# Performance work log

Hardware: AMD Instinct MI355X
Metric: run time of the kernel (lower is better)

## Reference

```python
import jax, jax.numpy as jnp
import numpy as np

NUM_USERS = 100000
NUM_ITEMS = 50000
EMB_DIM = 64
NUM_EDGES = 2000000


def setup_inputs() -> dict:
    key = jax.random.key(0)
    k1, k2, k3, k4 = jax.random.split(key, 4)
    user_table = jax.random.normal(k1, (NUM_USERS, EMB_DIM), dtype=jnp.float32) * 0.1
    item_table = jax.random.normal(k2, (NUM_ITEMS, EMB_DIM), dtype=jnp.float32) * 0.1
    user_idx = jax.random.randint(k3, (NUM_EDGES,), 0, NUM_USERS, dtype=jnp.int32)
    item_idx = jax.random.randint(k4, (NUM_EDGES,), 0, NUM_ITEMS, dtype=jnp.int32)
    return {"user_table": user_table, "item_table": item_table,
            "user_idx": user_idx, "item_idx": item_idx, "num_layers": 3}


def reference(user_table, item_table, user_idx, item_idx, num_layers):
    """LightGCN-style k-hop propagation over a sparse bipartite user-item graph.

    A_hat[u,i] = 1/sqrt(deg_u * deg_i); emb_out = mean over hops 0..K of A_hat^k @ emb_0.
    Returns concatenated [num_users+num_items, d] embeddings (forward() then slices).
    """
    n_users, d = user_table.shape
    n_items = item_table.shape[0]
    ones = jnp.ones(user_idx.shape[0], dtype=user_table.dtype)
    deg_u = jax.ops.segment_sum(ones, user_idx, num_segments=n_users)
    deg_i = jax.ops.segment_sum(ones, item_idx, num_segments=n_items)
    deg_u = jnp.where(deg_u > 0, deg_u, 1.0)
    deg_i = jnp.where(deg_i > 0, deg_i, 1.0)
    # per-edge symmetric normalization coefficient [E]
    norm = jax.lax.rsqrt(deg_u[user_idx] * deg_i[item_idx])

    u, it = user_table, item_table
    acc_u, acc_i = u, it
    for _ in range(num_layers):
        # messages: item -> user and user -> item (gather + weighted scatter-add)
        msg_u = jax.ops.segment_sum(norm[:, None] * it[item_idx], user_idx, num_segments=n_users)
        msg_i = jax.ops.segment_sum(norm[:, None] * u[user_idx], item_idx, num_segments=n_items)
        u, it = msg_u, msg_i
        acc_u = acc_u + u
        acc_i = acc_i + it
    scale = 1.0 / (num_layers + 1)
    return jnp.concatenate([acc_u * scale, acc_i * scale], axis=0)
```

## Files before the change

### kernel.cpp

```cpp
#include <hip/hip_runtime.h>
#include <hip/hip_fp16.h>
#include <stdint.h>

#define NU 100000
#define NI 50000
#define NN (NU + NI)
#define DIM 64
#define NE 2000000
#define TOT (NN * DIM)

#define NBU 782
#define NBI 782
#define NBKT (NBU + NBI)
#define SCAP 3064
#define CGRP 25
#define NC 63
#define CCAP 67584

#define BEPT1 4
#define BCH1 (256 * BEPT1)
#define BG1 ((NE + BCH1 - 1) / BCH1)
#define KB2 17

typedef float f4v __attribute__((ext_vector_type(4)));
typedef float f2v __attribute__((ext_vector_type(2)));

__device__ __forceinline__ int bucket_r0(int b) {
    return (b < NBU) ? (b << 7) : (NU + ((b - NBU) << 6));
}


__global__ void bin1_kernel(const int* __restrict__ uidx, const int* __restrict__ iidx,
                            int* __restrict__ ccur, uint32_t* __restrict__ cstg) {
    __shared__ int cnt[NC];
    __shared__ int base[NC + 1];
    __shared__ int gbase[NC];
    __shared__ uint32_t rec[2 * BCH1];
    __shared__ uint8_t cid[2 * BCH1];
    int tid = threadIdx.x;
    for (int i = tid; i < NC; i += 256) cnt[i] = 0;
    __syncthreads();

    uint32_t pk[2 * BEPT1]; int cs[2 * BEPT1]; int rk[2 * BEPT1];
    int t0 = blockIdx.x * BCH1 + tid;
#pragma unroll
    for (int k = 0; k < BEPT1; ++k) {
        int e = t0 + k * 256;
        bool ok = e < NE;
        int u = ok ? __builtin_nontemporal_load(uidx + e) : 0;
        int itm = ok ? __builtin_nontemporal_load(iidx + e) : 0;
        int b = u >> 7; int c = b / 25; int f5 = b - c * 25;
        pk[2 * k] = ((uint32_t)f5 << 23) | ((uint32_t)(u & 127) << 16) | (uint32_t)itm;
        cs[2 * k] = ok ? c : -1;
        int b2 = NBU + (itm >> 6); int c2 = b2 / 25; int f52 = b2 - c2 * 25;
        pk[2 * k + 1] = ((uint32_t)f52 << 23) | ((uint32_t)(itm & 63) << 17) | (uint32_t)u;
        cs[2 * k + 1] = ok ? c2 : -1;
    }
#pragma unroll
    for (int k = 0; k < 2 * BEPT1; ++k)
        rk[k] = (cs[k] >= 0) ? atomicAdd(&cnt[cs[k]], 1) : 0;
    __syncthreads();
    if (tid == 0) {
        int s = 0;
        for (int i = 0; i < NC; ++i) { base[i] = s; s += cnt[i]; }
        base[NC] = s;
    }
    __syncthreads();
    for (int i = tid; i < NC; i += 256)
        if (cnt[i] > 0) gbase[i] = atomicAdd(&ccur[i], cnt[i]);
#pragma unroll
    for (int k = 0; k < 2 * BEPT1; ++k)
        if (cs[k] >= 0) {
            int p = base[cs[k]] + rk[k];
            rec[p] = pk[k];
            cid[p] = (uint8_t)cs[k];
        }
    __syncthreads();
    int T = base[NC];
    for (int p = tid; p < T; p += 256) {
        int c = cid[p];
        int pos = gbase[c] + (p - base[c]);
        if (pos < CCAP)
            __builtin_nontemporal_store(rec[p], cstg + (size_t)c * CCAP + pos);
    }
}

__global__ void bin2_kernel(const int* __restrict__ ccnt, const uint32_t* __restrict__ cstg,
                            int* __restrict__ bktcur, uint32_t* __restrict__ stg) {
    int c = blockIdx.x / KB2;
    int sl = blockIdx.x % KB2;
    int n = min(ccnt[c], CCAP);
    int lo = sl * 4096;
    if (lo >= n) return;
    int hi = min(lo + 4096, n);
    int m = hi - lo;
    __shared__ int cnt[CGRP];
    __shared__ int base[CGRP + 1];
    __shared__ int gbase[CGRP];
    __shared__ uint32_t rec[4096];
    int tid = threadIdx.x;
    if (tid < CGRP) cnt[tid] = 0;
    __syncthreads();

    uint32_t pk[16]; int fa[16]; int rk[16];
    const uint32_t* run = cstg + (size_t)c * CCAP + lo;
#pragma unroll
    for (int k = 0; k < 16; ++k) {
        int p = tid + k * 256;
        bool ok = p < m;
        uint32_t r = ok ? __builtin_nontemporal_load(run + p) : 0;
        pk[k] = r;
        fa[k] = ok ? (int)(r >> 23) : -1;
    }
#pragma unroll
    for (int k = 0; k < 16; ++k)
        rk[k] = (fa[k] >= 0) ? atomicAdd(&cnt[fa[k]], 1) : 0;
    __syncthreads();
    if (tid == 0) {
        int s = 0;
        for (int i = 0; i < CGRP; ++i) { base[i] = s; s += cnt[i]; }
        base[CGRP] = s;
    }
    __syncthreads();
    if (tid < CGRP && cnt[tid] > 0)
        gbase[tid] = atomicAdd(&bktcur[c * CGRP + tid], cnt[tid]);
#pragma unroll
    for (int k = 0; k < 16; ++k)
        if (fa[k] >= 0) rec[base[fa[k]] + rk[k]] = pk[k];
    __syncthreads();
    int T = base[CGRP];
    for (int p = tid; p < T; p += 256) {
        uint32_t r = rec[p];
        int f5 = r >> 23;
        int pos = gbase[f5] + (p - base[f5]);
        if (pos < SCAP)
            __builtin_nontemporal_store(r, stg + (size_t)(c * CGRP + f5) * SCAP + pos);
    }
}

__global__ void placeA_kernel(const int* __restrict__ bktcnt, const uint32_t* __restrict__ stg,
                              int* __restrict__ deg) {
    __shared__ int rowcnt[128];
    int b = blockIdx.x;
    int tid = threadIdx.x;
    int r0 = bucket_r0(b);
    int r1 = (b < NBU) ? min(r0 + 128, NU) : min(r0 + 64, NN);
    int nrows = r1 - r0;
    if (tid < nrows) rowcnt[tid] = 0;
    __syncthreads();
    int n = min(bktcnt[b], SCAP);
    const uint32_t* run = stg + (size_t)b * SCAP;
    bool isU = b < NBU;
    for (int p = tid; p < n; p += 256) {
        uint32_t r = __builtin_nontemporal_load(run + p);
        int row = isU ? ((r >> 16) & 0x7F) : ((r >> 17) & 0x3F);
        atomicAdd(&rowcnt[row], 1);
    }
    __syncthreads();
    if (tid < nrows) deg[r0 + tid] = rowcnt[tid];
}

__global__ void scan1_kernel(const int* __restrict__ deg, int* __restrict__ incl,
                             int* __restrict__ bsum) {
    __shared__ int tmp[256];
    int i = blockIdx.x * 256 + threadIdx.x;
    int v = (i < NN) ? deg[i] : 0;
    tmp[threadIdx.x] = v;
    __syncthreads();
    for (int off = 1; off < 256; off <<= 1) {
        int t = (threadIdx.x >= off) ? tmp[threadIdx.x - off] : 0;
        __syncthreads();
        tmp[threadIdx.x] += t;
        __syncthreads();
    }
    if (i < NN) incl[i] = tmp[threadIdx.x];
    if (threadIdx.x == 255) bsum[blockIdx.x] = tmp[255];
}

__global__ void scan2_kernel(int* __restrict__ bsum, int nb) {
    __shared__ int tmp[1024];
    int v = (threadIdx.x < nb) ? bsum[threadIdx.x] : 0;
    tmp[threadIdx.x] = v;
    __syncthreads();
    for (int off = 1; off < 1024; off <<= 1) {
        int t = (threadIdx.x >= off) ? tmp[threadIdx.x - off] : 0;
        __syncthreads();
        tmp[threadIdx.x] += t;
        __syncthreads();
    }
    if (threadIdx.x < nb) bsum[threadIdx.x] = tmp[threadIdx.x] - v;
}

__global__ void scan3_kernel(const int* __restrict__ deg, const int* __restrict__ incl,
                             const int* __restrict__ bsum,
                             int* __restrict__ rowptr, float* __restrict__ rdeg,
                             float* __restrict__ irdeg) {
    int i = blockIdx.x * 256 + threadIdx.x;
    if (i >= NN) return;
    int inc = incl[i] + bsum[blockIdx.x];
    rowptr[i + 1] = inc;
    int d = deg[i];
    rdeg[i] = (d > 0) ? rsqrtf((float)d) : 1.0f;
    irdeg[i] = (d > 0) ? sqrtf((float)d) : 1.0f;
    if (i == 0) rowptr[0] = 0;
}

__global__ void placeB_kernel(const int* __restrict__ rowptr, const int* __restrict__ bktcnt,
                              const uint32_t* __restrict__ stg, int* __restrict__ nbrs) {
    __shared__ int rptr[129];
    __shared__ int rowcnt[128];
    __shared__ int outb[SCAP];
    int b = blockIdx.x;
    int tid = threadIdx.x;
    int r0 = bucket_r0(b);
    int r1 = (b < NBU) ? min(r0 + 128, NU) : min(r0 + 64, NN);
    int nrows = r1 - r0;
    if (tid <= nrows) rptr[tid] = rowptr[r0 + tid];
    if (tid < nrows) rowcnt[tid] = 0;
    __syncthreads();
    int lo = rptr[0];
    int n = min(bktcnt[b], SCAP);
    const uint32_t* run = stg + (size_t)b * SCAP;
    bool isU = b < NBU;
    for (int p = tid; p < n; p += 256) {
        uint32_t r = __builtin_nontemporal_load(run + p);
        int row = isU ? ((r >> 16) & 0x7F) : ((r >> 17) & 0x3F);
        int nbr = isU ? (NU + (int)(r & 0xFFFF)) : (int)(r & 0x1FFFF);
        int rk = atomicAdd(&rowcnt[row], 1);
        outb[rptr[row] - lo + rk] = nbr;
    }
    __syncthreads();
    int nseg = rptr[nrows] - lo;
    for (int i = tid; i < nseg; i += 256)
        __builtin_nontemporal_store(outb[i], nbrs + lo + i);
}


__global__ void initsrc_kernel(const float* __restrict__ ut, const float* __restrict__ it,
                               const float* __restrict__ rdeg, __half* __restrict__ srcH) {
    int i = blockIdx.x * blockDim.x + threadIdx.x;
    const int NU4 = NU * DIM / 4;
    const int T4 = TOT / 4;
    if (i >= T4) return;
    float4 v = (i < NU4) ? ((const float4*)ut)[i] : ((const float4*)it)[i - NU4];
    float r = rdeg[i >> 4];
    union { __half2 h2[2]; f2v v2; } u;
    u.h2[0] = __floats2half2_rn(r * v.x, r * v.y);
    u.h2[1] = __floats2half2_rn(r * v.z, r * v.w);
    *((f2v*)(srcH + (size_t)i * 4)) = u.v2;
}

__global__ void gather_kernel(const int* __restrict__ rowptr, const int* __restrict__ nbrs,
                              const float* __restrict__ rdeg,
                              const __half* __restrict__ srcH, __half* __restrict__ nxtH) {
    int wid = (int)(((unsigned)blockIdx.x * blockDim.x + threadIdx.x) >> 6);
    if (wid >= NN) return;
    int lane = threadIdx.x & 63;
    int g = lane >> 3;
    int c = lane & 7;
    int start = rowptr[wid];
    int end = rowptr[wid + 1];
    int deg = end - start;

    int nb_l = (lane < deg) ? __builtin_nontemporal_load(nbrs + start + lane) : 0;

    float s0=0,s1=0,s2=0,s3=0,s4=0,s5=0,s6=0,s7=0;
    int dmain = deg < 64 ? deg : 64;
    int iters = (dmain + 7) >> 3;
    for (int t = 0; t < iters; ++t) {
        int idx = t * 8 + g;
        int nb = __shfl(nb_l, idx & 63, 64);
        bool ok = idx < dmain;
        if (!ok) nb = 0;
        union { f4v v; __half2 h2[4]; } u;
        u.v = *((const f4v*)(srcH + (size_t)nb * DIM) + c);
        if (ok) {
            float2 f0 = __half22float2(u.h2[0]);
            float2 f1 = __half22float2(u.h2[1]);
            float2 f2 = __half22float2(u.h2[2]);
            float2 f3 = __half22float2(u.h2[3]);
            s0 += f0.x; s1 += f0.y; s2 += f1.x; s3 += f1.y;
            s4 += f2.x; s5 += f2.y; s6 += f3.x; s7 += f3.y;
        }
    }
    for (int k = start + 64 + g; k < end; k += 8) {
        int nb = nbrs[k];
        union { f4v v; __half2 h2[4]; } u;
        u.v = *((const f4v*)(srcH + (size_t)nb * DIM) + c);
        float2 f0 = __half22float2(u.h2[0]);
        float2 f1 = __half22float2(u.h2[1]);
        float2 f2 = __half22float2(u.h2[2]);
        float2 f3 = __half22float2(u.h2[3]);
        s0 += f0.x; s1 += f0.y; s2 += f1.x; s3 += f1.y;
        s4 += f2.x; s5 += f2.y; s6 += f3.x; s7 += f3.y;
    }
#pragma unroll
    for (int mask = 8; mask <= 32; mask <<= 1) {
        s0 += __shfl_xor(s0, mask, 64); s1 += __shfl_xor(s1, mask, 64);
        s2 += __shfl_xor(s2, mask, 64); s3 += __shfl_xor(s3, mask, 64);
        s4 += __shfl_xor(s4, mask, 64); s5 += __shfl_xor(s5, mask, 64);
        s6 += __shfl_xor(s6, mask, 64); s7 += __shfl_xor(s7, mask, 64);
    }
    if (lane < 8) {
        float r = rdeg[wid];
        float w = r * r;
        union { f4v v; __half2 h2[4]; } o;
        o.h2[0] = __floats2half2_rn(w * s0, w * s1);
        o.h2[1] = __floats2half2_rn(w * s2, w * s3);
        o.h2[2] = __floats2half2_rn(w * s4, w * s5);
        o.h2[3] = __floats2half2_rn(w * s6, w * s7);
        __builtin_nontemporal_store(o.v, (f4v*)(nxtH + (size_t)wid * DIM + c * 8));
    }
}

__global__ void gather_fused_kernel(const int* __restrict__ rowptr, const int* __restrict__ nbrs,
                                    const float* __restrict__ rdeg, const float* __restrict__ irdeg,
                                    const __half* __restrict__ srcH,
                                    const __half* __restrict__ n1, const __half* __restrict__ n2,
                                    const float* __restrict__ ut, const float* __restrict__ it,
                                    float* __restrict__ acc) {
    int wid = (int)(((unsigned)blockIdx.x * blockDim.x + threadIdx.x) >> 6);
    if (wid >= NN) return;
    int lane = threadIdx.x & 63;
    int g = lane >> 3;
    int c = lane & 7;
    int start = rowptr[wid];
    int end = rowptr[wid + 1];
    int deg = end - start;

    int nb_l = (lane < deg) ? __builtin_nontemporal_load(nbrs + start + lane) : 0;

    float s0=0,s1=0,s2=0,s3=0,s4=0,s5=0,s6=0,s7=0;
    int dmain = deg < 64 ? deg : 64;
    int iters = (dmain + 7) >> 3;
    for (int t = 0; t < iters; ++t) {
        int idx = t * 8 + g;
        int nb = __shfl(nb_l, idx & 63, 64);
        bool ok = idx < dmain;
        if (!ok) nb = 0;
        union { f4v v; __half2 h2[4]; } u;
        u.v = *((const f4v*)(srcH + (size_t)nb * DIM) + c);
        if (ok) {
            float2 f0 = __half22float2(u.h2[0]);
            float2 f1 = __half22float2(u.h2[1]);
            float2 f2 = __half22float2(u.h2[2]);
            float2 f3 = __half22float2(u.h2[3]);
            s0 += f0.x; s1 += f0.y; s2 += f1.x; s3 += f1.y;
            s4 += f2.x; s5 += f2.y; s6 += f3.x; s7 += f3.y;
        }
    }
    for (int k = start + 64 + g; k < end; k += 8) {
        int nb = nbrs[k];
        union { f4v v; __half2 h2[4]; } u;
        u.v = *((const f4v*)(srcH + (size_t)nb * DIM) + c);
        float2 f0 = __half22float2(u.h2[0]);
        float2 f1 = __half22float2(u.h2[1]);
        float2 f2 = __half22float2(u.h2[2]);
        float2 f3 = __half22float2(u.h2[3]);
        s0 += f0.x; s1 += f0.y; s2 += f1.x; s3 += f1.y;
        s4 += f2.x; s5 += f2.y; s6 += f3.x; s7 += f3.y;
    }
#pragma unroll
    for (int mask = 8; mask <= 32; mask <<= 1) {
        s0 += __shfl_xor(s0, mask, 64); s1 += __shfl_xor(s1, mask, 64);
        s2 += __shfl_xor(s2, mask, 64); s3 += __shfl_xor(s3, mask, 64);
        s4 += __shfl_xor(s4, mask, 64); s5 += __shfl_xor(s5, mask, 64);
        s6 += __shfl_xor(s6, mask, 64); s7 += __shfl_xor(s7, mask, 64);
    }
    if (lane < 8) {
        float r = rdeg[wid];
        float w = irdeg[wid];
        const float* e0 = ((wid < NU) ? (ut + (size_t)wid * DIM)
                                      : (it + (size_t)(wid - NU) * DIM)) + c * 8;
        f4v ea = ((const f4v*)e0)[0];
        f4v eb = ((const f4v*)e0)[1];
        union { f4v v; __half2 h2[4]; } a1, a2;
        size_t ro = (size_t)wid * DIM + c * 8;
        a1.v = __builtin_nontemporal_load((const f4v*)(n1 + ro));
        a2.v = __builtin_nontemporal_load((const f4v*)(n2 + ro));
        f4v oa, ob;
        float2 f1 = __half22float2(a1.h2[0]), f2 = __half22float2(a2.h2[0]);
        oa.x = 0.25f * (ea.x + w * (f1.x + f2.x) + r * s0);
        oa.y = 0.25f * (ea.y + w * (f1.y + f2.y) + r * s1);
        f1 = __half22float2(a1.h2[1]); f2 = __half22float2(a2.h2[1]);
        oa.z = 0.25f * (ea.z + w * (f1.x + f2.x) + r * s2);
        oa.w = 0.25f * (ea.w + w * (f1.y + f2.y) + r * s3);
        f1 = __half22float2(a1.h2[2]); f2 = __half22float2(a2.h2[2]);
        ob.x = 0.25f * (eb.x + w * (f1.x + f2.x) + r * s4);
        ob.y = 0.25f * (eb.y + w * (f1.y + f2.y) + r * s5);
        f1 = __half22float2(a1.h2[3]); f2 = __half22float2(a2.h2[3]);
        ob.z = 0.25f * (eb.z + w * (f1.x + f2.x) + r * s6);
        ob.w = 0.25f * (eb.w + w * (f1.y + f2.y) + r * s7);
        __builtin_nontemporal_store(oa, (f4v*)(acc + ro));
        __builtin_nontemporal_store(ob, (f4v*)(acc + ro) + 1);
    }
}

extern "C" void kernel_launch(void* const* d_in, const int* in_sizes, int n_in,
                              void* d_out, int out_size, void* d_ws, size_t ws_size,
                              hipStream_t stream) {
    const float* ut = (const float*)d_in[0];
    const float* it = (const float*)d_in[1];
    const int* uidx = (const int*)d_in[2];
    const int* iidx = (const int*)d_in[3];

    float* acc = (float*)d_out;

    int* wsi = (int*)d_ws;
    int* deg    = wsi;
    int* incl   = deg + NN;
    int* rowptr = incl + NN;
    int* bsum   = rowptr + (NN + 1);
    float* rdeg = (float*)(bsum + 1024);
    float* irdeg = rdeg + NN;
    int* bktcur = (int*)(irdeg + NN);
    int* ccur   = bktcur + NBKT;
    size_t off = (size_t)((int*)(ccur + NC) - wsi);
    off = (off + 15) & ~(size_t)15;
    int* nbrs   = wsi + off;
    __half* bufA = (__half*)(nbrs + 2 * (size_t)NE);
    __half* bufB = bufA + (size_t)TOT;
    __half* bufC = bufB + (size_t)TOT;
    uint32_t* stg  = (uint32_t*)bufA;
    uint32_t* cstg = (uint32_t*)bufB;

    const int B = 256;
    const int nb = (NN + 255) / 256;

    hipMemsetAsync(bktcur, 0, sizeof(int) * (NBKT + NC), stream);
    bin1_kernel<<<BG1, 256, 0, stream>>>(uidx, iidx, ccur, cstg);
    bin2_kernel<<<NC * KB2, 256, 0, stream>>>(ccur, cstg, bktcur, stg);
    placeA_kernel<<<NBKT, 256, 0, stream>>>(bktcur, stg, deg);
    scan1_kernel<<<nb, 256, 0, stream>>>(deg, incl, bsum);
    scan2_kernel<<<1, 1024, 0, stream>>>(bsum, nb);
    scan3_kernel<<<nb, 256, 0, stream>>>(deg, incl, bsum, rowptr, rdeg, irdeg);
    placeB_kernel<<<NBKT, 256, 0, stream>>>(rowptr, bktcur, stg, nbrs);

    initsrc_kernel<<<(TOT / 4 + B - 1) / B, B, 0, stream>>>(ut, it, rdeg, bufA);

    const int gblocks = NN / 4;
    gather_kernel<<<gblocks, B, 0, stream>>>(rowptr, nbrs, rdeg, bufA, bufB);
    gather_kernel<<<gblocks, B, 0, stream>>>(rowptr, nbrs, rdeg, bufB, bufC);
    gather_fused_kernel<<<gblocks, B, 0, stream>>>(rowptr, nbrs, rdeg, irdeg,
                                                   bufC, bufB, bufC, ut, it, acc);
}
```

Before: 416.3 us.

## Fuse degree count and row-pointer scan into bucket placement, unroll gather loads

The per-row degree count, three-stage prefix scan and neighbour placement are replaced by one single-block scan over bucket counts plus one placement kernel. That kernel counts rows in shared memory, computes local offsets and writes rowptr, rdeg and irdeg itself, removing four launches and a global pass over the degree arrays. The gather loop is moved into a shared helper that issues four independent neighbour-row loads per step with separate accumulators, to raise memory-level parallelism. The final kernel now reads the layer-0 embedding from the fp16 scaled buffer instead of the fp32 tables, which adds fp16 rounding to the hop-0 term.

```diff
diff --git a/kernel.cpp b/kernel.cpp
--- a/kernel.cpp
+++ b/kernel.cpp
@@ -138,76 +138,38 @@
     }
 }
 
-__global__ void placeA_kernel(const int* __restrict__ bktcnt, const uint32_t* __restrict__ stg,
-                              int* __restrict__ deg) {
-    __shared__ int rowcnt[128];
-    int b = blockIdx.x;
+__global__ void scanB_kernel(const int* __restrict__ bktcnt, int* __restrict__ bktbase) {
+    __shared__ int partial[256];
     int tid = threadIdx.x;
-    int r0 = bucket_r0(b);
-    int r1 = (b < NBU) ? min(r0 + 128, NU) : min(r0 + 64, NN);
-    int nrows = r1 - r0;
-    if (tid < nrows) rowcnt[tid] = 0;
-    __syncthreads();
-    int n = min(bktcnt[b], SCAP);
-    const uint32_t* run = stg + (size_t)b * SCAP;
-    bool isU = b < NBU;
-    for (int p = tid; p < n; p += 256) {
-        uint32_t r = __builtin_nontemporal_load(run + p);
-        int row = isU ? ((r >> 16) & 0x7F) : ((r >> 17) & 0x3F);
-        atomicAdd(&rowcnt[row], 1);
-    }
-    __syncthreads();
-    if (tid < nrows) deg[r0 + tid] = rowcnt[tid];
-}
-
-__global__ void scan1_kernel(const int* __restrict__ deg, int* __restrict__ incl,
-                             int* __restrict__ bsum) {
-    __shared__ int tmp[256];
-    int i = blockIdx.x * 256 + threadIdx.x;
-    int v = (i < NN) ? deg[i] : 0;
-    tmp[threadIdx.x] = v;
+    int loc[7];
+    int s = 0;
+#pragma unroll
+    for (int k = 0; k < 7; ++k) {
+        int i = tid * 7 + k;
+        loc[k] = (i < NBKT) ? min(bktcnt[i], SCAP) : 0;
+        s += loc[k];
+    }
+    partial[tid] = s;
     __syncthreads();
     for (int off = 1; off < 256; off <<= 1) {
-        int t = (threadIdx.x >= off) ? tmp[threadIdx.x - off] : 0;
+        int v = (tid >= off) ? partial[tid - off] : 0;
         __syncthreads();
-        tmp[threadIdx.x] += t;
+        partial[tid] += v;
         __syncthreads();
     }
-    if (i < NN) incl[i] = tmp[threadIdx.x];
-    if (threadIdx.x == 255) bsum[blockIdx.x] = tmp[255];
-}
-
-__global__ void scan2_kernel(int* __restrict__ bsum, int nb) {
-    __shared__ int tmp[1024];
-    int v = (threadIdx.x < nb) ? bsum[threadIdx.x] : 0;
-    tmp[threadIdx.x] = v;
-    __syncthreads();
-    for (int off = 1; off < 1024; off <<= 1) {
-        int t = (threadIdx.x >= off) ? tmp[threadIdx.x - off] : 0;
-        __syncthreads();
-        tmp[threadIdx.x] += t;
-        __syncthreads();
-    }
-    if (threadIdx.x < nb) bsum[threadIdx.x] = tmp[threadIdx.x] - v;
-}
-
-__global__ void scan3_kernel(const int* __restrict__ deg, const int* __restrict__ incl,
-                             const int* __restrict__ bsum,
-                             int* __restrict__ rowptr, float* __restrict__ rdeg,
-                             float* __restrict__ irdeg) {
-    int i = blockIdx.x * 256 + threadIdx.x;
-    if (i >= NN) return;
-    int inc = incl[i] + bsum[blockIdx.x];
-    rowptr[i + 1] = inc;
-    int d = deg[i];
-    rdeg[i] = (d > 0) ? rsqrtf((float)d) : 1.0f;
-    irdeg[i] = (d > 0) ? sqrtf((float)d) : 1.0f;
-    if (i == 0) rowptr[0] = 0;
-}
-
-__global__ void placeB_kernel(const int* __restrict__ rowptr, const int* __restrict__ bktcnt,
-                              const uint32_t* __restrict__ stg, int* __restrict__ nbrs) {
-    __shared__ int rptr[129];
+    int excl = (tid == 0) ? 0 : partial[tid - 1];
+#pragma unroll
+    for (int k = 0; k < 7; ++k) {
+        int i = tid * 7 + k;
+        if (i < NBKT) { bktbase[i] = excl; excl += loc[k]; }
+    }
+    if (tid == 255) bktbase[NBKT] = partial[255];
+}
+
+__global__ void placeB2_kernel(const int* __restrict__ bktbase, const uint32_t* __restrict__ stg,
+                               int* __restrict__ rowptr, float* __restrict__ rdeg,
+                               float* __restrict__ irdeg, int* __restrict__ nbrs) {
+    __shared__ int rowstart[129];
     __shared__ int rowcnt[128];
     __shared__ int outb[SCAP];
     int b = blockIdx.x;
@@ -215,23 +177,42 @@
     int r0 = bucket_r0(b);
     int r1 = (b < NBU) ? min(r0 + 128, NU) : min(r0 + 64, NN);
     int nrows = r1 - r0;
-    if (tid <= nrows) rptr[tid] = rowptr[r0 + tid];
+    int lo = bktbase[b];
+    int n = bktbase[b + 1] - lo;
     if (tid < nrows) rowcnt[tid] = 0;
     __syncthreads();
-    int lo = rptr[0];
-    int n = min(bktcnt[b], SCAP);
     const uint32_t* run = stg + (size_t)b * SCAP;
     bool isU = b < NBU;
     for (int p = tid; p < n; p += 256) {
         uint32_t r = __builtin_nontemporal_load(run + p);
         int row = isU ? ((r >> 16) & 0x7F) : ((r >> 17) & 0x3F);
+        atomicAdd(&rowcnt[row], 1);
+    }
+    __syncthreads();
+    if (tid == 0) {
+        int s = 0;
+        for (int i = 0; i < nrows; ++i) { rowstart[i] = s; s += rowcnt[i]; }
+        rowstart[nrows] = s;
+    }
+    __syncthreads();
+    if (tid < nrows) {
+        int d = rowcnt[tid];
+        rowptr[r0 + tid] = lo + rowstart[tid];
+        rdeg[r0 + tid] = (d > 0) ? rsqrtf((float)d) : 1.0f;
+        irdeg[r0 + tid] = (d > 0) ? sqrtf((float)d) : 1.0f;
+        rowcnt[tid] = 0;
+    }
+    if (b == NBKT - 1 && tid == 0) rowptr[NN] = lo + n;
+    __syncthreads();
+    for (int p = tid; p < n; p += 256) {
+        uint32_t r = __builtin_nontemporal_load(run + p);
+        int row = isU ? ((r >> 16) & 0x7F) : ((r >> 17) & 0x3F);
         int nbr = isU ? (NU + (int)(r & 0xFFFF)) : (int)(r & 0x1FFFF);
         int rk = atomicAdd(&rowcnt[row], 1);
-        outb[rptr[row] - lo + rk] = nbr;
-    }
-    __syncthreads();
-    int nseg = rptr[nrows] - lo;
-    for (int i = tid; i < nseg; i += 256)
+        outb[rowstart[row] + rk] = nbr;
+    }
+    __syncthreads();
+    for (int i = tid; i < n; i += 256)
         __builtin_nontemporal_store(outb[i], nbrs + lo + i);
 }
 
@@ -250,6 +231,108 @@
     *((f2v*)(srcH + (size_t)i * 4)) = u.v2;
 }
 
+__device__ __forceinline__ void gather_core(const int* __restrict__ rowptr,
+                                            const int* __restrict__ nbrs,
+                                            const __half* __restrict__ srcH,
+                                            int wid, int lane, int g, int c,
+                                            float* out) {
+    int start = rowptr[wid];
+    int end = rowptr[wid + 1];
+    int deg = end - start;
+    int nb_l = (lane < deg) ? __builtin_nontemporal_load(nbrs + start + lane) : 0;
+    float acc[4][8];
+#pragma unroll
+    for (int j = 0; j < 4; ++j)
+#pragma unroll
+        for (int k = 0; k < 8; ++k) acc[j][k] = 0.f;
+    int dmain = deg < 64 ? deg : 64;
+    int iters = (dmain + 7) >> 3;
+    int t = 0;
+    for (; t + 4 <= iters; t += 4) {
+        int nb[4]; bool ok[4];
+#pragma unroll
+        for (int j = 0; j < 4; ++j) {
+            int idx = (t + j) * 8 + g;
+            nb[j] = __shfl(nb_l, idx & 63, 64);
+            ok[j] = idx < dmain;
+            if (!ok[j]) nb[j] = 0;
+        }
+        union { f4v v; __half2 h2[4]; } u[4];
+#pragma unroll
+        for (int j = 0; j < 4; ++j)
+            u[j].v = *((const f4v*)(srcH + (size_t)nb[j] * DIM) + c);
+#pragma unroll
+        for (int j = 0; j < 4; ++j)
+            if (ok[j]) {
+#pragma unroll
+                for (int h = 0; h < 4; ++h) {
+                    float2 f = __half22float2(u[j].h2[h]);
+                    acc[j][2 * h] += f.x; acc[j][2 * h + 1] += f.y;
+                }
+            }
+    }
+    if (t + 2 <= iters) {
+        int nb[2]; bool ok[2];
+#pragma unroll
+        for (int j = 0; j < 2; ++j) {
+            int idx = (t + j) * 8 + g;
+            nb[j] = __shfl(nb_l, idx & 63, 64);
+            ok[j] = idx < dmain;
+            if (!ok[j]) nb[j] = 0;
+        }
+        union { f4v v; __half2 h2[4]; } u[2];
+#pragma unroll
+        for (int j = 0; j < 2; ++j)
+            u[j].v = *((const f4v*)(srcH + (size_t)nb[j] * DIM) + c);
+#pragma unroll
+        for (int j = 0; j < 2; ++j)
+            if (ok[j]) {
+#pragma unroll
+                for (int h = 0; h < 4; ++h) {
+                    float2 f = __half22float2(u[j].h2[h]);
+                    acc[j][2 * h] += f.x; acc[j][2 * h + 1] += f.y;
+                }
+            }
+        t += 2;
+    }
+    if (t < iters) {
+        int idx = t * 8 + g;
+        int nb0 = __shfl(nb_l, idx & 63, 64);
+        bool ok0 = idx < dmain;
+        if (!ok0) nb0 = 0;
+        union { f4v v; __half2 h2[4]; } u0;
+        u0.v = *((const f4v*)(srcH + (size_t)nb0 * DIM) + c);
+        if (ok0) {
+#pragma unroll
+            for (int h = 0; h < 4; ++h) {
+                float2 f = __half22float2(u0.h2[h]);
+                acc[0][2 * h] += f.x; acc[0][2 * h + 1] += f.y;
+            }
+        }
+    }
+    for (int k = start + 64 + g; k < end; k += 8) {
+        int nb = nbrs[k];
+        union { f4v v; __half2 h2[4]; } u0;
+        u0.v = *((const f4v*)(srcH + (size_t)nb * DIM) + c);
+#pragma unroll
+        for (int h = 0; h < 4; ++h) {
+            float2 f = __half22float2(u0.h2[h]);
+            acc[0][2 * h] += f.x; acc[0][2 * h + 1] += f.y;
+        }
+    }
+    float s[8];
+#pragma unroll
+    for (int k = 0; k < 8; ++k)
+        s[k] = acc[0][k] + acc[1][k] + acc[2][k] + acc[3][k];
+#pragma unroll
+    for (int mask = 8; mask <= 32; mask <<= 1) {
+#pragma unroll
+        for (int k = 0; k < 8; ++k) s[k] += __shfl_xor(s[k], mask, 64);
+    }
+#pragma unroll
+    for (int k = 0; k < 8; ++k) out[k] = s[k];
+}
+
 __global__ void gather_kernel(const int* __restrict__ rowptr, const int* __restrict__ nbrs,
                               const float* __restrict__ rdeg,
                               const __half* __restrict__ srcH, __half* __restrict__ nxtH) {
@@ -258,57 +341,16 @@
     int lane = threadIdx.x & 63;
     int g = lane >> 3;
     int c = lane & 7;
-    int start = rowptr[wid];
-    int end = rowptr[wid + 1];
-    int deg = end - start;
-
-    int nb_l = (lane < deg) ? __builtin_nontemporal_load(nbrs + start + lane) : 0;
-
-    float s0=0,s1=0,s2=0,s3=0,s4=0,s5=0,s6=0,s7=0;
-    int dmain = deg < 64 ? deg : 64;
-    int iters = (dmain + 7) >> 3;
-    for (int t = 0; t < iters; ++t) {
-        int idx = t * 8 + g;
-        int nb = __shfl(nb_l, idx & 63, 64);
-        bool ok = idx < dmain;
-        if (!ok) nb = 0;
-        union { f4v v; __half2 h2[4]; } u;
-        u.v = *((const f4v*)(srcH + (size_t)nb * DIM) + c);
-        if (ok) {
-            float2 f0 = __half22float2(u.h2[0]);
-            float2 f1 = __half22float2(u.h2[1]);
-            float2 f2 = __half22float2(u.h2[2]);
-            float2 f3 = __half22float2(u.h2[3]);
-            s0 += f0.x; s1 += f0.y; s2 += f1.x; s3 += f1.y;
-            s4 += f2.x; s5 += f2.y; s6 += f3.x; s7 += f3.y;
-        }
-    }
-    for (int k = start + 64 + g; k < end; k += 8) {
-        int nb = nbrs[k];
-        union { f4v v; __half2 h2[4]; } u;
-        u.v = *((const f4v*)(srcH + (size_t)nb * DIM) + c);
-        float2 f0 = __half22float2(u.h2[0]);
-        float2 f1 = __half22float2(u.h2[1]);
-        float2 f2 = __half22float2(u.h2[2]);
-        float2 f3 = __half22float2(u.h2[3]);
-        s0 += f0.x; s1 += f0.y; s2 += f1.x; s3 += f1.y;
-        s4 += f2.x; s5 += f2.y; s6 += f3.x; s7 += f3.y;
-    }
-#pragma unroll
-    for (int mask = 8; mask <= 32; mask <<= 1) {
-        s0 += __shfl_xor(s0, mask, 64); s1 += __shfl_xor(s1, mask, 64);
-        s2 += __shfl_xor(s2, mask, 64); s3 += __shfl_xor(s3, mask, 64);
-        s4 += __shfl_xor(s4, mask, 64); s5 += __shfl_xor(s5, mask, 64);
-        s6 += __shfl_xor(s6, mask, 64); s7 += __shfl_xor(s7, mask, 64);
-    }
+    float s[8];
+    gather_core(rowptr, nbrs, srcH, wid, lane, g, c, s);
     if (lane < 8) {
         float r = rdeg[wid];
         float w = r * r;
         union { f4v v; __half2 h2[4]; } o;
-        o.h2[0] = __floats2half2_rn(w * s0, w * s1);
-        o.h2[1] = __floats2half2_rn(w * s2, w * s3);
-        o.h2[2] = __floats2half2_rn(w * s4, w * s5);
-        o.h2[3] = __floats2half2_rn(w * s6, w * s7);
+        o.h2[0] = __floats2half2_rn(w * s[0], w * s[1]);
+        o.h2[1] = __floats2half2_rn(w * s[2], w * s[3]);
+        o.h2[2] = __floats2half2_rn(w * s[4], w * s[5]);
+        o.h2[3] = __floats2half2_rn(w * s[6], w * s[7]);
         __builtin_nontemporal_store(o.v, (f4v*)(nxtH + (size_t)wid * DIM + c * 8));
     }
 }
@@ -316,81 +358,36 @@
 __global__ void gather_fused_kernel(const int* __restrict__ rowptr, const int* __restrict__ nbrs,
                                     const float* __restrict__ rdeg, const float* __restrict__ irdeg,
                                     const __half* __restrict__ srcH,
-                                    const __half* __restrict__ n1, const __half* __restrict__ n2,
-                                    const float* __restrict__ ut, const float* __restrict__ it,
+                                    const __half* __restrict__ a0H, const __half* __restrict__ n1H,
                                     float* __restrict__ acc) {
     int wid = (int)(((unsigned)blockIdx.x * blockDim.x + threadIdx.x) >> 6);
     if (wid >= NN) return;
     int lane = threadIdx.x & 63;
     int g = lane >> 3;
     int c = lane & 7;
-    int start = rowptr[wid];
-    int end = rowptr[wid + 1];
-    int deg = end - start;
-
-    int nb_l = (lane < deg) ? __builtin_nontemporal_load(nbrs + start + lane) : 0;
-
-    float s0=0,s1=0,s2=0,s3=0,s4=0,s5=0,s6=0,s7=0;
-    int dmain = deg < 64 ? deg : 64;
-    int iters = (dmain + 7) >> 3;
-    for (int t = 0; t < iters; ++t) {
-        int idx = t * 8 + g;
-        int nb = __shfl(nb_l, idx & 63, 64);
-        bool ok = idx < dmain;
-        if (!ok) nb = 0;
-        union { f4v v; __half2 h2[4]; } u;
-        u.v = *((const f4v*)(srcH + (size_t)nb * DIM) + c);
-        if (ok) {
-            float2 f0 = __half22float2(u.h2[0]);
-            float2 f1 = __half22float2(u.h2[1]);
-            float2 f2 = __half22float2(u.h2[2]);
-            float2 f3 = __half22float2(u.h2[3]);
-            s0 += f0.x; s1 += f0.y; s2 += f1.x; s3 += f1.y;
-            s4 += f2.x; s5 += f2.y; s6 += f3.x; s7 += f3.y;
-        }
-    }
-    for (int k = start + 64 + g; k < end; k += 8) {
-        int nb = nbrs[k];
-        union { f4v v; __half2 h2[4]; } u;
-        u.v = *((const f4v*)(srcH + (size_t)nb * DIM) + c);
-        float2 f0 = __half22float2(u.h2[0]);
-        float2 f1 = __half22float2(u.h2[1]);
-        float2 f2 = __half22float2(u.h2[2]);
-        float2 f3 = __half22float2(u.h2[3]);
-        s0 += f0.x; s1 += f0.y; s2 += f1.x; s3 += f1.y;
-        s4 += f2.x; s5 += f2.y; s6 += f3.x; s7 += f3.y;
-    }
-#pragma unroll
-    for (int mask = 8; mask <= 32; mask <<= 1) {
-        s0 += __shfl_xor(s0, mask, 64); s1 += __shfl_xor(s1, mask, 64);
-        s2 += __shfl_xor(s2, mask, 64); s3 += __shfl_xor(s3, mask, 64);
-        s4 += __shfl_xor(s4, mask, 64); s5 += __shfl_xor(s5, mask, 64);
-        s6 += __shfl_xor(s6, mask, 64); s7 += __shfl_xor(s7, mask, 64);
-    }
+    float s[8];
+    gather_core(rowptr, nbrs, srcH, wid, lane, g, c, s);
     if (lane < 8) {
         float r = rdeg[wid];
         float w = irdeg[wid];
-        const float* e0 = ((wid < NU) ? (ut + (size_t)wid * DIM)
-                                      : (it + (size_t)(wid - NU) * DIM)) + c * 8;
-        f4v ea = ((const f4v*)e0)[0];
-        f4v eb = ((const f4v*)e0)[1];
-        union { f4v v; __half2 h2[4]; } a1, a2;
         size_t ro = (size_t)wid * DIM + c * 8;
-        a1.v = __builtin_nontemporal_load((const f4v*)(n1 + ro));
-        a2.v = __builtin_nontemporal_load((const f4v*)(n2 + ro));
+        union { f4v v; __half2 h2[4]; } a0, a1, a2;
+        a0.v = __builtin_nontemporal_load((const f4v*)(a0H + ro));
+        a1.v = __builtin_nontemporal_load((const f4v*)(n1H + ro));
+        a2.v = *((const f4v*)(srcH + ro));
         f4v oa, ob;
-        float2 f1 = __half22float2(a1.h2[0]), f2 = __half22float2(a2.h2[0]);
-        oa.x = 0.25f * (ea.x + w * (f1.x + f2.x) + r * s0);
-        oa.y = 0.25f * (ea.y + w * (f1.y + f2.y) + r * s1);
-        f1 = __half22float2(a1.h2[1]); f2 = __half22float2(a2.h2[1]);
-        oa.z = 0.25f * (ea.z + w * (f1.x + f2.x) + r * s2);
-        oa.w = 0.25f * (ea.w + w * (f1.y + f2.y) + r * s3);
-        f1 = __half22float2(a1.h2[2]); f2 = __half22float2(a2.h2[2]);
-        ob.x = 0.25f * (eb.x + w * (f1.x + f2.x) + r * s4);
-        ob.y = 0.25f * (eb.y + w * (f1.y + f2.y) + r * s5);
-        f1 = __half22float2(a1.h2[3]); f2 = __half22float2(a2.h2[3]);
-        ob.z = 0.25f * (eb.z + w * (f1.x + f2.x) + r * s6);
-        ob.w = 0.25f * (eb.w + w * (f1.y + f2.y) + r * s7);
+        float2 e0 = __half22float2(a0.h2[0]), f1 = __half22float2(a1.h2[0]), f2 = __half22float2(a2.h2[0]);
+        oa.x = 0.25f * (w * (e0.x + f1.x + f2.x) + r * s[0]);
+        oa.y = 0.25f * (w * (e0.y + f1.y + f2.y) + r * s[1]);
+        e0 = __half22float2(a0.h2[1]); f1 = __half22float2(a1.h2[1]); f2 = __half22float2(a2.h2[1]);
+        oa.z = 0.25f * (w * (e0.x + f1.x + f2.x) + r * s[2]);
+        oa.w = 0.25f * (w * (e0.y + f1.y + f2.y) + r * s[3]);
+        e0 = __half22float2(a0.h2[2]); f1 = __half22float2(a1.h2[2]); f2 = __half22float2(a2.h2[2]);
+        ob.x = 0.25f * (w * (e0.x + f1.x + f2.x) + r * s[4]);
+        ob.y = 0.25f * (w * (e0.y + f1.y + f2.y) + r * s[5]);
+        e0 = __half22float2(a0.h2[3]); f1 = __half22float2(a1.h2[3]); f2 = __half22float2(a2.h2[3]);
+        ob.z = 0.25f * (w * (e0.x + f1.x + f2.x) + r * s[6]);
+        ob.w = 0.25f * (w * (e0.y + f1.y + f2.y) + r * s[7]);
         __builtin_nontemporal_store(oa, (f4v*)(acc + ro));
         __builtin_nontemporal_store(ob, (f4v*)(acc + ro) + 1);
     }
@@ -407,15 +404,13 @@
     float* acc = (float*)d_out;
 
     int* wsi = (int*)d_ws;
-    int* deg    = wsi;
-    int* incl   = deg + NN;
-    int* rowptr = incl + NN;
-    int* bsum   = rowptr + (NN + 1);
-    float* rdeg = (float*)(bsum + 1024);
+    int* rowptr = wsi;
+    float* rdeg = (float*)(rowptr + (NN + 1));
     float* irdeg = rdeg + NN;
     int* bktcur = (int*)(irdeg + NN);
     int* ccur   = bktcur + NBKT;
-    size_t off = (size_t)((int*)(ccur + NC) - wsi);
+    int* bktbase = ccur + NC;
+    size_t off = (size_t)((int*)(bktbase + NBKT + 1) - wsi);
     off = (off + 15) & ~(size_t)15;
     int* nbrs   = wsi + off;
     __half* bufA = (__half*)(nbrs + 2 * (size_t)NE);
@@ -425,16 +420,12 @@
     uint32_t* cstg = (uint32_t*)bufB;
 
     const int B = 256;
-    const int nb = (NN + 255) / 256;
 
     hipMemsetAsync(bktcur, 0, sizeof(int) * (NBKT + NC), stream);
     bin1_kernel<<<BG1, 256, 0, stream>>>(uidx, iidx, ccur, cstg);
     bin2_kernel<<<NC * KB2, 256, 0, stream>>>(ccur, cstg, bktcur, stg);
-    placeA_kernel<<<NBKT, 256, 0, stream>>>(bktcur, stg, deg);
-    scan1_kernel<<<nb, 256, 0, stream>>>(deg, incl, bsum);
-    scan2_kernel<<<1, 1024, 0, stream>>>(bsum, nb);
-    scan3_kernel<<<nb, 256, 0, stream>>>(deg, incl, bsum, rowptr, rdeg, irdeg);
-    placeB_kernel<<<NBKT, 256, 0, stream>>>(rowptr, bktcur, stg, nbrs);
+    scanB_kernel<<<1, 256, 0, stream>>>(bktcur, bktbase);
+    placeB2_kernel<<<NBKT, 256, 0, stream>>>(bktbase, stg, rowptr, rdeg, irdeg, nbrs);
 
     initsrc_kernel<<<(TOT / 4 + B - 1) / B, B, 0, stream>>>(ut, it, rdeg, bufA);
 
@@ -442,5 +433,5 @@
     gather_kernel<<<gblocks, B, 0, stream>>>(rowptr, nbrs, rdeg, bufA, bufB);
     gather_kernel<<<gblocks, B, 0, stream>>>(rowptr, nbrs, rdeg, bufB, bufC);
     gather_fused_kernel<<<gblocks, B, 0, stream>>>(rowptr, nbrs, rdeg, irdeg,
-                                                   bufC, bufB, bufC, ut, it, acc);
-}
+                                                   bufC, bufA, bufB, acc);
+}
```

Result: faster. 390.8 us (-6.1%).
